# Performance work log

Hardware: AMD Instinct MI355X
Metric: run time of the kernel (lower is better)

Reference implementation:

```python
import jax, jax.numpy as jnp
import numpy as np

DIM = 256
FEAT = 768
KVQ = 256
H = 4
DH = KVQ // H
ITERS = 3
EPS = 1e-8
SCALE = DH ** -0.5


def _ln(x, g, b):
    m = jnp.mean(x, axis=-1, keepdims=True)
    v = jnp.var(x, axis=-1, keepdims=True)
    return (x - m) / jnp.sqrt(v + 1e-5) * g + b


def setup_inputs() -> dict:
    key = jax.random.key(0)
    ks = jax.random.split(key, 16)
    p = lambda k, shape: (jax.random.normal(k, shape, dtype=jnp.float32) * 0.02)
    return {
        "inputs": jax.random.normal(ks[0], (32, 4096, FEAT), dtype=jnp.float32),
        "conditioning": jax.random.normal(ks[1], (32, 16, DIM), dtype=jnp.float32),
        "to_q_w": p(ks[2], (KVQ, DIM)),
        "to_k_w": p(ks[3], (KVQ, FEAT)),
        "to_v_w": p(ks[4], (KVQ, FEAT)),
        "gru_w_ih": p(ks[5], (3 * DIM, KVQ)),
        "gru_w_hh": p(ks[6], (3 * DIM, DIM)),
        "gru_b_ih": jnp.zeros((3 * DIM,), jnp.float32),
        "gru_b_hh": jnp.zeros((3 * DIM,), jnp.float32),
        "ln_in_g": jnp.ones((FEAT,), jnp.float32),
        "ln_in_b": jnp.zeros((FEAT,), jnp.float32),
        "ln_slots_g": jnp.ones((DIM,), jnp.float32),
        "ln_slots_b": jnp.zeros((DIM,), jnp.float32),
        "ff_ln_g": jnp.ones((DIM,), jnp.float32),
        "ff_ln_b": jnp.zeros((DIM,), jnp.float32),
        "ff_w1": p(ks[7], (4 * DIM, DIM)),
        "ff_b1": jnp.zeros((4 * DIM,), jnp.float32),
        "ff_w2": p(ks[8], (DIM, 4 * DIM)),
        "ff_b2": jnp.zeros((DIM,), jnp.float32),
    }


def _gru(x, h, w_ih, w_hh, b_ih, b_hh):
    # PyTorch GRUCell: gates ordered (r, z, n)
    gi = x @ w_ih.T + b_ih
    gh = h @ w_hh.T + b_hh
    gi_r, gi_z, gi_n = jnp.split(gi, 3, axis=-1)
    gh_r, gh_z, gh_n = jnp.split(gh, 3, axis=-1)
    r = jax.nn.sigmoid(gi_r + gh_r)
    z = jax.nn.sigmoid(gi_z + gh_z)
    n = jnp.tanh(gi_n + r * gh_n)
    return (1.0 - z) * n + z * h


def reference(inputs, conditioning, to_q_w, to_k_w, to_v_w, gru_w_ih, gru_w_hh,
              gru_b_ih, gru_b_hh, ln_in_g, ln_in_b, ln_slots_g, ln_slots_b,
              ff_ln_g, ff_ln_b, ff_w1, ff_b1, ff_w2, ff_b2):
    B, N, _ = inputs.shape
    K = conditioning.shape[1]
    x = _ln(inputs, ln_in_g, ln_in_b)
    k = (x @ to_k_w.T).reshape(B, N, H, DH)
    v = (x @ to_v_w.T).reshape(B, N, H, DH)

    slots = conditioning
    attn_out = None
    for _ in range(ITERS):
        slots_prev = slots
        s = _ln(slots, ln_slots_g, ln_slots_b)
        q = (s @ to_q_w.T).reshape(B, K, H, DH)
        dots = jnp.einsum('bihd,bjhd->bihj', q, k) * SCALE  # [B,K,H,N]
        # softmax jointly over slots*heads
        attn = jax.nn.softmax(dots.reshape(B, K * H, N), axis=1).reshape(B, K, H, N)
        attn_out = attn.mean(axis=2)  # [B,K,N]
        w = attn + EPS
        w = w / jnp.sum(w, axis=-1, keepdims=True)
        updates = jnp.einsum('bjhd,bihj->bihd', v, w).reshape(B * K, KVQ)
        slots = _gru(updates, slots_prev.reshape(B * K, DIM),
                     gru_w_ih, gru_w_hh, gru_b_ih, gru_b_hh).reshape(B, K, DIM)
        h = _ln(slots, ff_ln_g, ff_ln_b)
        h = jax.nn.gelu(h @ ff_w1.T + ff_b1, approximate=False) @ ff_w2.T + ff_b2
        slots = slots + h
    return slots, attn_out
```

## Files before the change

### kernel.cpp

```cpp
#include <hip/hip_runtime.h>

#define B_SZ 32
#define N_TOK 4096
#define FEAT 768
#define DIM 256
#define NSLOT 16
#define NH 4
#define DH 64
#define M_TOKENS 131072
#define SCALE 0.125f
#define EPS_ATTN 1e-8f
#define MCHUNK 32768

typedef unsigned short u16;
typedef __attribute__((ext_vector_type(8))) short short8;
typedef __attribute__((ext_vector_type(4))) float floatx4;

__device__ __forceinline__ u16 f2bf(float f) {
    unsigned int u = __float_as_uint(f);
    u += 0x7FFFu + ((u >> 16) & 1u);
    return (u16)(u >> 16);
}
__device__ __forceinline__ float bf2f(u16 u) {
    return __uint_as_float(((unsigned int)u) << 16);
}
__device__ __forceinline__ void gl_lds16(const void* g, void* l) {
    __builtin_amdgcn_global_load_lds((const __attribute__((address_space(1))) void*)g,
                                     (__attribute__((address_space(3))) void*)l, 16, 0, 0);
}
__device__ __forceinline__ float sigm(float x) { return 1.f / (1.f + expf(-x)); }

template<int TK, int EPI>
__global__ __launch_bounds__(256) void gemm_bt(
    const u16* __restrict__ A0, const u16* __restrict__ A1,
    const u16* __restrict__ B0, const u16* __restrict__ B1,
    void* __restrict__ C0, void* __restrict__ C1,
    const float* __restrict__ bias, const float* __restrict__ res,
    float* __restrict__ out2, int ldc) {
    __shared__ u16 As[128 * 32];
    __shared__ u16 Bs[128 * 32];
    int t = threadIdx.x, w = t >> 6, lane = t & 63;
    int n0 = blockIdx.x * 128;
    size_t m0 = (size_t)blockIdx.y * 128;
    const u16* A = (blockIdx.z && A1) ? A1 : A0;
    const u16* B = (blockIdx.z && B1) ? B1 : B0;

    floatx4 acc[2][8];
#pragma unroll
    for (int mt = 0; mt < 2; ++mt)
#pragma unroll
        for (int nt = 0; nt < 8; ++nt) acc[mt][nt] = (floatx4)(0.f);

    int srow = (lane >> 2), seg = lane & 3;
    for (int k0 = 0; k0 < TK; k0 += 32) {
#pragma unroll
        for (int c = 0; c < 2; ++c) {
            int row = w * 32 + c * 16 + srow;
            gl_lds16(A + (m0 + row) * TK + k0 + seg * 8, &As[(w * 32 + c * 16) * 32]);
            gl_lds16(B + (size_t)(n0 + row) * TK + k0 + seg * 8, &Bs[(w * 32 + c * 16) * 32]);
        }
        __syncthreads();
        short8 af[2];
#pragma unroll
        for (int mt = 0; mt < 2; ++mt)
            af[mt] = *(const short8*)&As[(w * 32 + mt * 16 + (lane & 15)) * 32 + (lane >> 4) * 8];
        short8 bfr[8];
#pragma unroll
        for (int nt = 0; nt < 8; ++nt)
            bfr[nt] = *(const short8*)&Bs[(nt * 16 + (lane & 15)) * 32 + (lane >> 4) * 8];
#pragma unroll
        for (int mt = 0; mt < 2; ++mt)
#pragma unroll
            for (int nt = 0; nt < 8; ++nt)
                acc[mt][nt] = __builtin_amdgcn_mfma_f32_16x16x32_bf16(af[mt], bfr[nt], acc[mt][nt], 0, 0, 0);
        __syncthreads();
    }
#pragma unroll
    for (int mt = 0; mt < 2; ++mt)
#pragma unroll
        for (int nt = 0; nt < 8; ++nt)
#pragma unroll
            for (int rr = 0; rr < 4; ++rr) {
                size_t row = m0 + w * 32 + mt * 16 + (lane >> 4) * 4 + rr;
                int col = n0 + nt * 16 + (lane & 15);
                float v = acc[mt][nt][rr];
                if (EPI == 0) {
                    if (col < 256) ((u16*)C0)[row * 256 + col] = f2bf(v);
                    else           ((u16*)C1)[row * 256 + col - 256] = f2bf(v);
                } else if (EPI == 1) {
                    ((u16*)C0)[row * (size_t)ldc + col] = f2bf(v);
                } else if (EPI == 2) {
                    float* Cf = (float*)(blockIdx.z ? C1 : C0);
                    Cf[row * (size_t)ldc + col] = v;
                } else if (EPI == 3) {
                    float a = v + bias[col];
                    float g = 0.5f * a * (1.f + erff(a * 0.70710678118654752f));
                    ((u16*)C0)[row * (size_t)ldc + col] = f2bf(g);
                } else if (EPI == 4) {
                    float a = v + bias[col] + res[row * 256 + col];
                    ((float*)C0)[row * 256 + col] = a;
                    out2[row * 256 + col] = a;
                }
            }
}

__global__ __launch_bounds__(256) void k_ln_bf16(const float* __restrict__ x,
                                                 const float* __restrict__ lg,
                                                 const float* __restrict__ lb,
                                                 u16* __restrict__ xln) {
    int w = threadIdx.x >> 6, lane = threadIdx.x & 63;
    size_t row = (size_t)blockIdx.x * 4 + w;
    const float4* x4 = (const float4*)(x + row * FEAT);
    float4 a[3];
    float s = 0.f, sq = 0.f;
#pragma unroll
    for (int p = 0; p < 3; ++p) {
        a[p] = x4[p * 64 + lane];
        s += a[p].x + a[p].y + a[p].z + a[p].w;
        sq += a[p].x * a[p].x + a[p].y * a[p].y + a[p].z * a[p].z + a[p].w * a[p].w;
    }
#pragma unroll
    for (int off = 32; off >= 1; off >>= 1) {
        s += __shfl_xor(s, off);
        sq += __shfl_xor(sq, off);
    }
    float m = s * (1.f / 768.f);
    float rs = rsqrtf(sq * (1.f / 768.f) - m * m + 1e-5f);
#pragma unroll
    for (int p = 0; p < 3; ++p) {
        float4 g = *(const float4*)(lg + (p * 64 + lane) * 4);
        float4 b = *(const float4*)(lb + (p * 64 + lane) * 4);
        ushort4 o;
        o.x = f2bf((a[p].x - m) * rs * g.x + b.x);
        o.y = f2bf((a[p].y - m) * rs * g.y + b.y);
        o.z = f2bf((a[p].z - m) * rs * g.z + b.z);
        o.w = f2bf((a[p].w - m) * rs * g.w + b.w);
        *(ushort4*)(xln + row * FEAT + (p * 64 + lane) * 4) = o;
    }
}

#define OFF_WKV 0
#define OFF_WQ  393216
#define OFF_WIH 458752
#define OFF_WHH 655360
#define OFF_W1  851968
#define OFF_W2  1114112
#define W_TOTAL 1376256
__global__ __launch_bounds__(256) void k_wcvt(
    const float* __restrict__ wk, const float* __restrict__ wv,
    const float* __restrict__ wq, const float* __restrict__ wih,
    const float* __restrict__ whh, const float* __restrict__ w1,
    const float* __restrict__ w2, u16* __restrict__ wall) {
    int base = (blockIdx.x * 256 + threadIdx.x) * 4;
    if (base >= W_TOTAL) return;
#pragma unroll
    for (int q = 0; q < 4; ++q) {
        int id = base + q;
        float v;
        if (id < OFF_WQ) {
            int r = id / 768, c = id - r * 768;
            v = (r < 256) ? wk[r * 768 + c] : wv[(r - 256) * 768 + c];
        } else if (id < OFF_WIH) v = wq[id - OFF_WQ] * SCALE;
        else if (id < OFF_W1)    v = (id < OFF_WHH) ? wih[id - OFF_WIH] : whh[id - OFF_WHH];
        else if (id < OFF_W2)    v = w1[id - OFF_W1];
        else                     v = w2[id - OFF_W2];
        wall[id] = f2bf(v);
    }
}

__global__ __launch_bounds__(256) void k_vt(const u16* __restrict__ vb,
                                            u16* __restrict__ vt) {
    __shared__ u16 lds[256 * 66];
    int t = threadIdx.x;
    int b = blockIdx.y, j0 = blockIdx.x * 64;
#pragma unroll
    for (int it = 0; it < 16; ++it) {
        int flat = it * 256 + t;
        int j = flat >> 6, c4 = flat & 63;
        ushort4 vv = *(const ushort4*)(vb + ((size_t)b * 4096 + j0 + j) * 256 + c4 * 4);
        lds[(c4 * 4 + 0) * 66 + j] = vv.x;
        lds[(c4 * 4 + 1) * 66 + j] = vv.y;
        lds[(c4 * 4 + 2) * 66 + j] = vv.z;
        lds[(c4 * 4 + 3) * 66 + j] = vv.w;
    }
    __syncthreads();
#pragma unroll
    for (int it = 0; it < 8; ++it) {
        int flat = it * 256 + t;
        int d = flat >> 3, jseg = flat & 7;
        const unsigned int* s32 = (const unsigned int*)(lds + d * 66 + jseg * 8);
        uint4 o;
        o.x = s32[0]; o.y = s32[1]; o.z = s32[2]; o.w = s32[3];
        *(uint4*)(vt + ((size_t)b * 256 + d) * 4096 + j0 + jseg * 8) = o;
    }
}

__global__ __launch_bounds__(256) void k_vsum(const u16* __restrict__ vt,
                                              float* __restrict__ vsum) {
    int w = threadIdx.x >> 6, lane = threadIdx.x & 63;
    int r = blockIdx.x * 4 + w;
    const short8* row = (const short8*)(vt + (size_t)r * 4096);
    float s = 0.f;
#pragma unroll
    for (int it = 0; it < 8; ++it) {
        union { short8 v; u16 e[8]; } u;
        u.v = row[it * 64 + lane];
#pragma unroll
        for (int q = 0; q < 8; ++q) s += bf2f(u.e[q]);
    }
#pragma unroll
    for (int off = 32; off >= 1; off >>= 1) s += __shfl_xor(s, off);
    if (lane == 0) vsum[r] = s;
}

__global__ __launch_bounds__(256) void k_slots_ln(const float* __restrict__ sp,
                                                  const float* __restrict__ lg,
                                                  const float* __restrict__ lb,
                                                  u16* __restrict__ sln, u16* __restrict__ hpb,
                                                  float* __restrict__ sums) {
    int t = threadIdx.x, w = t >> 6, lane = t & 63;
    if (blockIdx.x < 8) sums[blockIdx.x * 256 + t] = 0.f;
    int r = blockIdx.x * 4 + w;
    float4 v = *(const float4*)(sp + (size_t)r * 256 + lane * 4);
    float s1 = v.x + v.y + v.z + v.w;
    float s2 = v.x * v.x + v.y * v.y + v.z * v.z + v.w * v.w;
#pragma unroll
    for (int off = 32; off >= 1; off >>= 1) {
        s1 += __shfl_xor(s1, off);
        s2 += __shfl_xor(s2, off);
    }
    float m = s1 * (1.f / 256.f);
    float rs = rsqrtf(s2 * (1.f / 256.f) - m * m + 1e-5f);
    float4 g = *(const float4*)(lg + lane * 4);
    float4 b = *(const float4*)(lb + lane * 4);
    ushort4 o, hp;
    o.x = f2bf((v.x - m) * rs * g.x + b.x); o.y = f2bf((v.y - m) * rs * g.y + b.y);
    o.z = f2bf((v.z - m) * rs * g.z + b.z); o.w = f2bf((v.w - m) * rs * g.w + b.w);
    hp.x = f2bf(v.x); hp.y = f2bf(v.y); hp.z = f2bf(v.z); hp.w = f2bf(v.w);
    *(ushort4*)(sln + (size_t)r * 256 + lane * 4) = o;
    *(ushort4*)(hpb + (size_t)r * 256 + lane * 4) = hp;
}

__global__ __launch_bounds__(256) void k_dots(const u16* __restrict__ qb,
                                              const u16* __restrict__ kb,
                                              const u16* __restrict__ vt,
                                              float* __restrict__ part,
                                              float* __restrict__ sums,
                                              float* __restrict__ out_attn, int last) {
    __shared__ float dots_s[64 * 65];
    __shared__ float attn_s[64 * 65];
    __shared__ float aout_s[64 * 16];
    int t = threadIdx.x, w = t >> 6, lane = t & 63;
    int b = blockIdx.y, jb = blockIdx.x, j0 = jb * 64;
    int h = w, i15 = lane & 15, qq = lane >> 4;

    short8 afq[2];
#pragma unroll
    for (int kf = 0; kf < 2; ++kf)
        afq[kf] = *(const short8*)(qb + (size_t)(b * 16 + i15) * 256 + h * 64 + kf * 32 + qq * 8);
#pragma unroll
    for (int jt = 0; jt < 4; ++jt) {
        floatx4 acc = (floatx4)(0.f);
#pragma unroll
        for (int kf = 0; kf < 2; ++kf) {
            short8 bf = *(const short8*)(kb + ((size_t)b * 4096 + j0 + jt * 16 + i15) * 256 + h * 64 + kf * 32 + qq * 8);
            acc = __builtin_amdgcn_mfma_f32_16x16x32_bf16(afq[kf], bf, acc, 0, 0, 0);
        }
#pragma unroll
        for (int r = 0; r < 4; ++r)
            dots_s[(jt * 16 + i15) * 65 + h * 16 + qq * 4 + r] = acc[r];
    }
    __syncthreads();
    float ssum = 0.f;
#pragma unroll
    for (int jj = 0; jj < 16; ++jj) {
        int jl = w * 16 + jj;
        float d = dots_s[jl * 65 + lane];
        float mx = d;
#pragma unroll
        for (int off = 32; off >= 1; off >>= 1) mx = fmaxf(mx, __shfl_xor(mx, off));
        float e = __expf(d - mx);
        float sm = e;
#pragma unroll
        for (int off = 32; off >= 1; off >>= 1) sm += __shfl_xor(sm, off);
        float a = e / sm;
        attn_s[jl * 65 + lane] = a;
        ssum += a;
        if (last) {
            float am = a + __shfl_xor(a, 16);
            am += __shfl_xor(am, 32);
            if (lane < 16) aout_s[jl * 16 + lane] = am * 0.25f;
        }
    }
    atomicAdd(&sums[b * 64 + lane], ssum);
    __syncthreads();
    short8 afa[2];
#pragma unroll
    for (int kf = 0; kf < 2; ++kf) {
        union { short8 s; u16 e[8]; } u;
#pragma unroll
        for (int jj = 0; jj < 8; ++jj)
            u.e[jj] = f2bf(attn_s[(kf * 32 + qq * 8 + jj) * 65 + h * 16 + i15]);
        afa[kf] = u.s;
    }
#pragma unroll
    for (int nt = 0; nt < 4; ++nt) {
        floatx4 acc = (floatx4)(0.f);
#pragma unroll
        for (int kf = 0; kf < 2; ++kf) {
            short8 bf = *(const short8*)(vt + ((size_t)b * 256 + h * 64 + nt * 16 + i15) * 4096 + j0 + kf * 32 + qq * 8);
            acc = __builtin_amdgcn_mfma_f32_16x16x32_bf16(afa[kf], bf, acc, 0, 0, 0);
        }
#pragma unroll
        for (int r = 0; r < 4; ++r)
            part[((size_t)b * 64 + jb) * 4096 + h * 1024 + (qq * 4 + r) * 64 + nt * 16 + i15] = acc[r];
    }
    if (last) {
        __syncthreads();
        int i = t >> 4, jq4 = (t & 15) * 4;
        float4 v;
        v.x = aout_s[(jq4 + 0) * 16 + i];
        v.y = aout_s[(jq4 + 1) * 16 + i];
        v.z = aout_s[(jq4 + 2) * 16 + i];
        v.w = aout_s[(jq4 + 3) * 16 + i];
        *(float4*)(out_attn + ((size_t)b * 16 + i) * 4096 + j0 + jq4) = v;
    }
}

__global__ __launch_bounds__(256) void k_ured(const float* __restrict__ part,
                                              const float* __restrict__ sums,
                                              const float* __restrict__ vsum,
                                              u16* __restrict__ ub) {
    int r = blockIdx.x, t = threadIdx.x;
    int b = r >> 4;
    int c = (r & 15) * 256 + t;
    const float* pb = part + (size_t)b * 64 * 4096 + c;
    float acc = 0.f;
#pragma unroll 16
    for (int jb = 0; jb < 64; ++jb) acc += pb[(size_t)jb * 4096];
    int h = c >> 10, i = (c >> 6) & 15, d = c & 63;
    float rinv = 1.f / (sums[b * 64 + h * 16 + i] + 4096.f * EPS_ATTN);
    float vs = vsum[b * 256 + h * 64 + d];
    ub[((size_t)b * 16 + i) * 256 + h * 64 + d] = f2bf((acc + EPS_ATTN * vs) * rinv);
}

__global__ __launch_bounds__(256) void k_gates(const float* __restrict__ gi,
                                               const float* __restrict__ gh,
                                               const float* __restrict__ sp,
                                               const float* __restrict__ bih,
                                               const float* __restrict__ bhh,
                                               const float* __restrict__ ffg,
                                               const float* __restrict__ ffb,
                                               float* __restrict__ hn_ws,
                                               u16* __restrict__ hln) {
    int t = threadIdx.x, w = t >> 6, lane = t & 63;
    int r = blockIdx.x * 4 + w;
    const float4* gi4 = (const float4*)(gi + (size_t)r * 768);
    const float4* gh4 = (const float4*)(gh + (size_t)r * 768);
    const float4* bi4 = (const float4*)bih;
    const float4* bh4 = (const float4*)bhh;
    float4 gir = gi4[lane], giz = gi4[64 + lane], gin = gi4[128 + lane];
    float4 ghr = gh4[lane], ghz = gh4[64 + lane], ghn = gh4[128 + lane];
    float4 bir = bi4[lane], biz = bi4[64 + lane], bin = bi4[128 + lane];
    float4 bhr = bh4[lane], bhz = bh4[64 + lane], bhn = bh4[128 + lane];
    float4 hp = *(const float4*)(sp + (size_t)r * 256 + lane * 4);
    float4 hn;
    {
        float rg, zg, ng;
        rg = sigm(gir.x + bir.x + ghr.x + bhr.x); zg = sigm(giz.x + biz.x + ghz.x + bhz.x);
        ng = tanhf(gin.x + bin.x + rg * (ghn.x + bhn.x)); hn.x = (1.f - zg) * ng + zg * hp.x;
        rg = sigm(gir.y + bir.y + ghr.y + bhr.y); zg = sigm(giz.y + biz.y + ghz.y + bhz.y);
        ng = tanhf(gin.y + bin.y + rg * (ghn.y + bhn.y)); hn.y = (1.f - zg) * ng + zg * hp.y;
        rg = sigm(gir.z + bir.z + ghr.z + bhr.z); zg = sigm(giz.z + biz.z + ghz.z + bhz.z);
        ng = tanhf(gin.z + bin.z + rg * (ghn.z + bhn.z)); hn.z = (1.f - zg) * ng + zg * hp.z;
        rg = sigm(gir.w + bir.w + ghr.w + bhr.w); zg = sigm(giz.w + biz.w + ghz.w + bhz.w);
        ng = tanhf(gin.w + bin.w + rg * (ghn.w + bhn.w)); hn.w = (1.f - zg) * ng + zg * hp.w;
    }
    *(float4*)(hn_ws + (size_t)r * 256 + lane * 4) = hn;
    float s1 = hn.x + hn.y + hn.z + hn.w;
    float s2 = hn.x * hn.x + hn.y * hn.y + hn.z * hn.z + hn.w * hn.w;
#pragma unroll
    for (int off = 32; off >= 1; off >>= 1) {
        s1 += __shfl_xor(s1, off);
        s2 += __shfl_xor(s2, off);
    }
    float m = s1 * (1.f / 256.f);
    float rs = rsqrtf(s2 * (1.f / 256.f) - m * m + 1e-5f);
    float4 g = *(const float4*)(ffg + lane * 4);
    float4 b = *(const float4*)(ffb + lane * 4);
    ushort4 o;
    o.x = f2bf((hn.x - m) * rs * g.x + b.x); o.y = f2bf((hn.y - m) * rs * g.y + b.y);
    o.z = f2bf((hn.z - m) * rs * g.z + b.z); o.w = f2bf((hn.w - m) * rs * g.w + b.w);
    *(ushort4*)(hln + (size_t)r * 256 + lane * 4) = o;
}

extern "C" void kernel_launch(void* const* d_in, const int* in_sizes, int n_in,
                              void* d_out, int out_size, void* d_ws, size_t ws_size,
                              hipStream_t stream) {
    const float* inputs   = (const float*)d_in[0];
    const float* cond     = (const float*)d_in[1];
    const float* to_q_w   = (const float*)d_in[2];
    const float* to_k_w   = (const float*)d_in[3];
    const float* to_v_w   = (const float*)d_in[4];
    const float* gru_w_ih = (const float*)d_in[5];
    const float* gru_w_hh = (const float*)d_in[6];
    const float* gru_b_ih = (const float*)d_in[7];
    const float* gru_b_hh = (const float*)d_in[8];
    const float* ln_in_g  = (const float*)d_in[9];
    const float* ln_in_b  = (const float*)d_in[10];
    const float* ln_sl_g  = (const float*)d_in[11];
    const float* ln_sl_b  = (const float*)d_in[12];
    const float* ff_ln_g  = (const float*)d_in[13];
    const float* ff_ln_b  = (const float*)d_in[14];
    const float* ff_w1    = (const float*)d_in[15];
    const float* ff_b1    = (const float*)d_in[16];
    const float* ff_w2    = (const float*)d_in[17];
    const float* ff_b2    = (const float*)d_in[18];

    float* out_slots = (float*)d_out;
    float* out_attn  = (float*)d_out + 131072;

    char* p = (char*)d_ws;
    u16* kbuf = (u16*)p;                  p += (size_t)M_TOKENS * 256 * 2;
    char* vregion = p;                    p += (size_t)M_TOKENS * 256 * 2;
    u16*   vbuf = (u16*)vregion;
    float* part = (float*)vregion;
    float* gi   = (float*)(vregion + 33554432);
    float* gh   = (float*)(vregion + 35127296);
    char* tregion = p;                    p += (size_t)M_TOKENS * 256 * 2;
    u16* xln_c = (u16*)tregion;
    u16* vT    = (u16*)tregion;
    u16* wall = (u16*)p;                  p += (size_t)W_TOTAL * 2;
    u16* qbuf = (u16*)p;                  p += 131072 * 2;
    u16* sln  = (u16*)p;                  p += 131072 * 2;
    u16* hpb  = (u16*)p;                  p += 131072 * 2;
    u16* ub   = (u16*)p;                  p += 131072 * 2;
    u16* hln  = (u16*)p;                  p += 131072 * 2;
    u16* g1   = (u16*)p;                  p += (size_t)512 * 1024 * 2;
    float* slots_ws = (float*)p;          p += 131072 * 4;
    float* hn_ws    = (float*)p;          p += 131072 * 4;
    float* sums     = (float*)p;          p += 2048 * 4;
    float* vsum     = (float*)p;          p += 8192 * 4;

    k_wcvt<<<(W_TOTAL / 4 + 255) / 256, 256, 0, stream>>>(
        to_k_w, to_v_w, to_q_w, gru_w_ih, gru_w_hh, ff_w1, ff_w2, wall);

    for (int c = 0; c < 4; ++c) {
        k_ln_bf16<<<MCHUNK / 4, 256, 0, stream>>>(
            inputs + (size_t)c * MCHUNK * FEAT, ln_in_g, ln_in_b, xln_c);
        gemm_bt<768, 0><<<dim3(4, MCHUNK / 128, 1), 256, 0, stream>>>(
            xln_c, nullptr, wall + OFF_WKV, nullptr,
            kbuf + (size_t)c * MCHUNK * 256, vbuf + (size_t)c * MCHUNK * 256,
            nullptr, nullptr, nullptr, 256);
    }
    k_vt<<<dim3(64, 32), 256, 0, stream>>>(vbuf, vT);
    k_vsum<<<2048 / 4 * 4 / 4, 256, 0, stream>>>(vT, vsum);

    for (int it = 0; it < 3; ++it) {
        const float* sp = (it == 0) ? cond : slots_ws;
        int last = (it == 2) ? 1 : 0;
        k_slots_ln<<<128, 256, 0, stream>>>(sp, ln_sl_g, ln_sl_b, sln, hpb, sums);
        gemm_bt<256, 1><<<dim3(2, 4, 1), 256, 0, stream>>>(
            sln, nullptr, wall + OFF_WQ, nullptr, qbuf, nullptr, nullptr, nullptr, nullptr, 256);
        k_dots<<<dim3(64, 32), 256, 0, stream>>>(qbuf, kbuf, vT, part, sums, out_attn, last);
        k_ured<<<512, 256, 0, stream>>>(part, sums, vsum, ub);
        gemm_bt<256, 2><<<dim3(6, 4, 2), 256, 0, stream>>>(
            ub, hpb, wall + OFF_WIH, wall + OFF_WHH, gi, gh, nullptr, nullptr, nullptr, 768);
        k_gates<<<128, 256, 0, stream>>>(gi, gh, sp, gru_b_ih, gru_b_hh,
                                         ff_ln_g, ff_ln_b, hn_ws, hln);
        gemm_bt<256, 3><<<dim3(8, 4, 1), 256, 0, stream>>>(
            hln, nullptr, wall + OFF_W1, nullptr, g1, nullptr, ff_b1, nullptr, nullptr, 1024);
        gemm_bt<1024, 4><<<dim3(2, 4, 1), 256, 0, stream>>>(
            g1, nullptr, wall + OFF_W2, nullptr, slots_ws, nullptr, ff_b2, hn_ws,
            last ? out_slots : slots_ws, 256);
    }
}
```

Baseline: 1.127 ms.

## Fuse V transpose and V column-sum into KV projection GEMM epilogue

The KV projection GEMM now writes V directly in transposed layout through an LDS staging buffer and accumulates per-column V sums with atomics, replacing the separate transpose and vsum kernels. The four-chunk LN+GEMM loop becomes a single full-size launch with a larger xln buffer, and the block index is remapped so consecutive workgroups fan out across token rows. vsum is zeroed inside the weight-convert kernel. This removes a full read and write of V plus extra launches, at the cost of more workspace, extra epilogue work and float atomics that make vsum order-nondeterministic.

```diff
diff --git a/kernel.cpp b/kernel.cpp
--- a/kernel.cpp
+++ b/kernel.cpp
@@ -10,7 +10,6 @@
 #define M_TOKENS 131072
 #define SCALE 0.125f
 #define EPS_ATTN 1e-8f
-#define MCHUNK 32768
 
 typedef unsigned short u16;
 typedef __attribute__((ext_vector_type(8))) short short8;
@@ -37,11 +36,22 @@
     void* __restrict__ C0, void* __restrict__ C1,
     const float* __restrict__ bias, const float* __restrict__ res,
     float* __restrict__ out2, int ldc) {
-    __shared__ u16 As[128 * 32];
-    __shared__ u16 Bs[128 * 32];
+    __shared__ union SMem {
+        u16 ab[2][128 * 32];
+        u16 tr[64 * 136];
+    } sm;
+    u16* As = sm.ab[0];
+    u16* Bs = sm.ab[1];
     int t = threadIdx.x, w = t >> 6, lane = t & 63;
-    int n0 = blockIdx.x * 128;
-    size_t m0 = (size_t)blockIdx.y * 128;
+    int bx = blockIdx.x, by = blockIdx.y;
+    if (EPI == 0) {
+        int flat = by * 4 + bx;
+        int lg = (flat & 7) * 512 + (flat >> 3);
+        by = lg >> 2;
+        bx = lg & 3;
+    }
+    int n0 = bx * 128;
+    size_t m0 = (size_t)by * 128;
     const u16* A = (blockIdx.z && A1) ? A1 : A0;
     const u16* B = (blockIdx.z && B1) ? B1 : B0;
 
@@ -75,6 +85,41 @@
                 acc[mt][nt] = __builtin_amdgcn_mfma_f32_16x16x32_bf16(af[mt], bfr[nt], acc[mt][nt], 0, 0, 0);
         __syncthreads();
     }
+
+    if (EPI == 0 && n0 >= 256) {
+        int tok0 = (int)m0;
+        int b = tok0 >> 12, jb0 = tok0 & 4095;
+        int cb = n0 - 256;
+        u16* vt = (u16*)C1;
+#pragma unroll
+        for (int pass = 0; pass < 2; ++pass) {
+            __syncthreads();
+#pragma unroll
+            for (int mt = 0; mt < 2; ++mt)
+#pragma unroll
+                for (int q = 0; q < 4; ++q) {
+                    int nt = pass * 4 + q;
+#pragma unroll
+                    for (int rr = 0; rr < 4; ++rr) {
+                        int row = w * 32 + mt * 16 + (lane >> 4) * 4 + rr;
+                        sm.tr[(q * 16 + (lane & 15)) * 136 + row] = f2bf(acc[mt][nt][rr]);
+                    }
+                }
+            __syncthreads();
+            int cl = t >> 2, js = (t & 3) * 32;
+            const u16* src = &sm.tr[cl * 136 + js];
+            float s = 0.f;
+#pragma unroll
+            for (int qi = 0; qi < 32; ++qi) s += bf2f(src[qi]);
+            u16* dst = vt + ((size_t)(b * 256 + cb + pass * 64 + cl)) * 4096 + jb0 + js;
+#pragma unroll
+            for (int qi = 0; qi < 4; ++qi)
+                *(uint4*)(dst + qi * 8) = *(const uint4*)(src + qi * 8);
+            atomicAdd(&out2[b * 256 + cb + pass * 64 + cl], s);
+        }
+        return;
+    }
+
 #pragma unroll
     for (int mt = 0; mt < 2; ++mt)
 #pragma unroll
@@ -85,8 +130,7 @@
                 int col = n0 + nt * 16 + (lane & 15);
                 float v = acc[mt][nt][rr];
                 if (EPI == 0) {
-                    if (col < 256) ((u16*)C0)[row * 256 + col] = f2bf(v);
-                    else           ((u16*)C1)[row * 256 + col - 256] = f2bf(v);
+                    ((u16*)C0)[row * 256 + col] = f2bf(v);
                 } else if (EPI == 1) {
                     ((u16*)C0)[row * (size_t)ldc + col] = f2bf(v);
                 } else if (EPI == 2) {
@@ -150,7 +194,12 @@
     const float* __restrict__ wk, const float* __restrict__ wv,
     const float* __restrict__ wq, const float* __restrict__ wih,
     const float* __restrict__ whh, const float* __restrict__ w1,
-    const float* __restrict__ w2, u16* __restrict__ wall) {
+    const float* __restrict__ w2, u16* __restrict__ wall,
+    float* __restrict__ vsum) {
+    if (blockIdx.x < 8) {
+        float4 z; z.x = z.y = z.z = z.w = 0.f;
+        *(float4*)(vsum + ((size_t)blockIdx.x * 256 + threadIdx.x) * 4) = z;
+    }
     int base = (blockIdx.x * 256 + threadIdx.x) * 4;
     if (base >= W_TOTAL) return;
 #pragma unroll
@@ -166,51 +215,6 @@
         else                     v = w2[id - OFF_W2];
         wall[id] = f2bf(v);
     }
-}
-
-__global__ __launch_bounds__(256) void k_vt(const u16* __restrict__ vb,
-                                            u16* __restrict__ vt) {
-    __shared__ u16 lds[256 * 66];
-    int t = threadIdx.x;
-    int b = blockIdx.y, j0 = blockIdx.x * 64;
-#pragma unroll
-    for (int it = 0; it < 16; ++it) {
-        int flat = it * 256 + t;
-        int j = flat >> 6, c4 = flat & 63;
-        ushort4 vv = *(const ushort4*)(vb + ((size_t)b * 4096 + j0 + j) * 256 + c4 * 4);
-        lds[(c4 * 4 + 0) * 66 + j] = vv.x;
-        lds[(c4 * 4 + 1) * 66 + j] = vv.y;
-        lds[(c4 * 4 + 2) * 66 + j] = vv.z;
-        lds[(c4 * 4 + 3) * 66 + j] = vv.w;
-    }
-    __syncthreads();
-#pragma unroll
-    for (int it = 0; it < 8; ++it) {
-        int flat = it * 256 + t;
-        int d = flat >> 3, jseg = flat & 7;
-        const unsigned int* s32 = (const unsigned int*)(lds + d * 66 + jseg * 8);
-        uint4 o;
-        o.x = s32[0]; o.y = s32[1]; o.z = s32[2]; o.w = s32[3];
-        *(uint4*)(vt + ((size_t)b * 256 + d) * 4096 + j0 + jseg * 8) = o;
-    }
-}
-
-__global__ __launch_bounds__(256) void k_vsum(const u16* __restrict__ vt,
-                                              float* __restrict__ vsum) {
-    int w = threadIdx.x >> 6, lane = threadIdx.x & 63;
-    int r = blockIdx.x * 4 + w;
-    const short8* row = (const short8*)(vt + (size_t)r * 4096);
-    float s = 0.f;
-#pragma unroll
-    for (int it = 0; it < 8; ++it) {
-        union { short8 v; u16 e[8]; } u;
-        u.v = row[it * 64 + lane];
-#pragma unroll
-        for (int q = 0; q < 8; ++q) s += bf2f(u.e[q]);
-    }
-#pragma unroll
-    for (int off = 32; off >= 1; off >>= 1) s += __shfl_xor(s, off);
-    if (lane == 0) vsum[r] = s;
 }
 
 __global__ __launch_bounds__(256) void k_slots_ln(const float* __restrict__ sp,
@@ -422,14 +426,12 @@
 
     char* p = (char*)d_ws;
     u16* kbuf = (u16*)p;                  p += (size_t)M_TOKENS * 256 * 2;
-    char* vregion = p;                    p += (size_t)M_TOKENS * 256 * 2;
-    u16*   vbuf = (u16*)vregion;
-    float* part = (float*)vregion;
-    float* gi   = (float*)(vregion + 33554432);
-    float* gh   = (float*)(vregion + 35127296);
+    u16* vT   = (u16*)p;                  p += (size_t)M_TOKENS * 256 * 2;
     char* tregion = p;                    p += (size_t)M_TOKENS * 256 * 2;
-    u16* xln_c = (u16*)tregion;
-    u16* vT    = (u16*)tregion;
+    float* part = (float*)tregion;
+    float* gi   = (float*)(tregion + 33554432);
+    float* gh   = (float*)(tregion + 35127296);
+    u16* xln  = (u16*)p;                  p += (size_t)M_TOKENS * FEAT * 2;
     u16* wall = (u16*)p;                  p += (size_t)W_TOTAL * 2;
     u16* qbuf = (u16*)p;                  p += 131072 * 2;
     u16* sln  = (u16*)p;                  p += 131072 * 2;
@@ -443,18 +445,12 @@
     float* vsum     = (float*)p;          p += 8192 * 4;
 
     k_wcvt<<<(W_TOTAL / 4 + 255) / 256, 256, 0, stream>>>(
-        to_k_w, to_v_w, to_q_w, gru_w_ih, gru_w_hh, ff_w1, ff_w2, wall);
-
-    for (int c = 0; c < 4; ++c) {
-        k_ln_bf16<<<MCHUNK / 4, 256, 0, stream>>>(
-            inputs + (size_t)c * MCHUNK * FEAT, ln_in_g, ln_in_b, xln_c);
-        gemm_bt<768, 0><<<dim3(4, MCHUNK / 128, 1), 256, 0, stream>>>(
-            xln_c, nullptr, wall + OFF_WKV, nullptr,
-            kbuf + (size_t)c * MCHUNK * 256, vbuf + (size_t)c * MCHUNK * 256,
-            nullptr, nullptr, nullptr, 256);
-    }
-    k_vt<<<dim3(64, 32), 256, 0, stream>>>(vbuf, vT);
-    k_vsum<<<2048 / 4 * 4 / 4, 256, 0, stream>>>(vT, vsum);
+        to_k_w, to_v_w, to_q_w, gru_w_ih, gru_w_hh, ff_w1, ff_w2, wall, vsum);
+
+    k_ln_bf16<<<M_TOKENS / 4, 256, 0, stream>>>(inputs, ln_in_g, ln_in_b, xln);
+    gemm_bt<768, 0><<<dim3(4, M_TOKENS / 128, 1), 256, 0, stream>>>(
+        xln, nullptr, wall + OFF_WKV, nullptr,
+        kbuf, vT, nullptr, nullptr, vsum, 0);
 
     for (int it = 0; it < 3; ++it) {
         const float* sp = (it == 0) ? cond : slots_ws;
```

After: 1.238 ms. +9.8%, slower.
